# Kernel optimization log

Measured on AMD Instinct MI355X. Metric: run time of the kernel, lower is better.

The kernel has to match this reference:

```python
import jax, jax.numpy as jnp
import numpy as np
from jax import lax

LR, SB, LB = 256, 16, 8  # lr_size, spatial_bin, luma_bins
DN = ('NCHW', 'OIHW', 'NCHW')


def conv2d(x, w, b=None, stride=1, pad=1):
    out = lax.conv_general_dilated(x, w, (stride, stride), [(pad, pad), (pad, pad)], dimension_numbers=DN)
    return out if b is None else out + b[None, :, None, None]


def gaussian_blur17(x):
    # kornia GaussianBlur2d(kernel=(17,17), sigma=(2,2)), reflect padding, separable
    t = jnp.arange(17, dtype=x.dtype) - 8.0
    g = jnp.exp(-(t * t) / 8.0)  # 2*sigma^2 = 8
    g = g / g.sum()
    C = x.shape[1]
    xp = jnp.pad(x, ((0, 0), (0, 0), (8, 8), (8, 8)), mode='reflect')
    kh = jnp.broadcast_to(g.reshape(1, 1, 17, 1), (C, 1, 17, 1))
    kw = jnp.broadcast_to(g.reshape(1, 1, 1, 17), (C, 1, 1, 17))
    x1 = lax.conv_general_dilated(xp, kh, (1, 1), 'VALID', dimension_numbers=DN, feature_group_count=C)
    return lax.conv_general_dilated(x1, kw, (1, 1), 'VALID', dimension_numbers=DN, feature_group_count=C)


def nearest_resize(x, size):
    # torch F.interpolate mode='nearest': src = floor(dst * in/out)
    H, W = x.shape[-2], x.shape[-1]
    iy = jnp.floor(jnp.arange(size) * (H / size)).astype(jnp.int32)
    ix = jnp.floor(jnp.arange(size) * (W / size)).astype(jnp.int32)
    return x[:, :, iy][:, :, :, ix]


def grid_sample_3d_border(inp, grid):
    # inp [B,C,D,Hi,Wi]; grid [B,Do,Ho,Wo,3] with (x,y,z); bilinear, padding_mode='border', align_corners=False
    B, C, D, Hi, Wi = inp.shape
    x = jnp.clip(((grid[..., 0] + 1.0) * Wi - 1.0) * 0.5, 0.0, Wi - 1.0)
    y = jnp.clip(((grid[..., 1] + 1.0) * Hi - 1.0) * 0.5, 0.0, Hi - 1.0)
    z = jnp.clip(((grid[..., 2] + 1.0) * D - 1.0) * 0.5, 0.0, D - 1.0)
    x0 = jnp.floor(x); y0 = jnp.floor(y); z0 = jnp.floor(z)
    fx = (x - x0)[:, None]; fy = (y - y0)[:, None]; fz = (z - z0)[:, None]  # [B,1,Do,Ho,Wo]
    x0i = x0.astype(jnp.int32); y0i = y0.astype(jnp.int32); z0i = z0.astype(jnp.int32)
    x1i = jnp.minimum(x0i + 1, Wi - 1); y1i = jnp.minimum(y0i + 1, Hi - 1); z1i = jnp.minimum(z0i + 1, D - 1)
    flat = inp.reshape(B, C, D * Hi * Wi)
    M = grid.shape[1] * grid.shape[2] * grid.shape[3]

    def gat(zi, yi, xi):
        idx = ((zi * Hi + yi) * Wi + xi).reshape(B, 1, M)
        v = jnp.take_along_axis(flat, jnp.broadcast_to(idx, (B, C, M)), axis=2)
        return v.reshape(B, C, grid.shape[1], grid.shape[2], grid.shape[3])

    return (gat(z0i, y0i, x0i) * (1 - fz) * (1 - fy) * (1 - fx)
            + gat(z0i, y0i, x1i) * (1 - fz) * (1 - fy) * fx
            + gat(z0i, y1i, x0i) * (1 - fz) * fy * (1 - fx)
            + gat(z0i, y1i, x1i) * (1 - fz) * fy * fx
            + gat(z1i, y0i, x0i) * fz * (1 - fy) * (1 - fx)
            + gat(z1i, y0i, x1i) * fz * (1 - fy) * fx
            + gat(z1i, y1i, x0i) * fz * fy * (1 - fx)
            + gat(z1i, y1i, x1i) * fz * fy * fx)


def _forward(lqs, evs, gw1, gb1, gw2, gb2, sw0, sb0, sw1, sb1, sw2, sb2, sw3, sb3,
             cw0, cb0, cw1, cb1, fw1, fb1, fw2, fb2, fw3, fb3, lw1, lb1, lw2, fuw, fub):
    B, _, H, W = lqs.shape
    # --- HighresStreamNet guide ---
    g = gaussian_blur17(lqs)
    g = jax.nn.relu(conv2d(g, gw1, gb1, 1, 0))
    guide = jax.nn.sigmoid(conv2d(g, gw2, gb2, 1, 0)) * 2.0 - 0.5  # [B,1,H,W]
    # --- slicing grid (x,y in (-0.5,1.5) per source, z = guide) ---
    gx = (jnp.arange(W, dtype=lqs.dtype) + 0.5) / W * 2.0 - 0.5
    gy = (jnp.arange(H, dtype=lqs.dtype) + 0.5) / H * 2.0 - 0.5
    gyy, gxx = jnp.meshgrid(gy, gx, indexing='ij')
    base = jnp.broadcast_to(jnp.stack([gxx, gyy], -1)[None, None], (B, 1, H, W, 2))
    grid = jnp.concatenate([base, guide[..., None]], axis=-1)  # [B,1,H,W,3]
    # --- LowresStreamNet ---
    lr = nearest_resize(lqs, LR)
    ev = evs if (evs.shape[-1] == LR and evs.shape[-2] == LR) else nearest_resize(evs, LR)
    x = jnp.concatenate([lr, ev], axis=1)  # [B,18,256,256]
    for w_, b_ in ((sw0, sb0), (sw1, sb1), (sw2, sb2), (sw3, sb3)):
        x = jax.nn.relu(conv2d(x, w_, b_, 2, 1))  # -> [B,64,16,16]
    xl = conv2d(jax.nn.relu(conv2d(x, lw1, lb1, 1, 1)), lw2, None, 1, 1)  # local, last conv no bias
    xg = jax.nn.relu(conv2d(x, cw0, cb0, 2, 1))
    xg = jax.nn.relu(conv2d(xg, cw1, cb1, 2, 1)).reshape(B, -1)  # [B,1024]
    xg = jax.nn.relu(xg @ fw1.T + fb1)
    xg = jax.nn.relu(xg @ fw2.T + fb2)
    xg = xg @ fw3.T + fb3  # [B,64]
    fused = jax.nn.relu(xg[:, :, None, None] + xl)
    bg = conv2d(fused, fuw, fub, 1, 0).reshape(B, 1, LB, SB, SB)  # bilateral grid [B,1,8,16,16]
    hr = grid_sample_3d_border(bg, grid)  # [B,1,1,H,W]
    return hr.reshape(B, -1, H, W)


def setup_inputs():
    key = jax.random.key(0)
    ks = iter(jax.random.split(key, 40))

    def W_(shape):
        fan_in = int(np.prod(shape[1:]))
        return jax.random.normal(next(ks), shape, jnp.float32) * np.float32(np.sqrt(2.0 / fan_in))

    def Z(n):
        return jnp.zeros((n,), jnp.float32)

    B, H, Wd = 8, 1024, 1024
    return {
        'lqs': jax.random.uniform(next(ks), (B, 3, H, Wd), jnp.float32),
        'evs': jax.random.normal(next(ks), (B, 15, 256, 256), jnp.float32) * 0.1,
        'gw1': W_((16, 3, 1, 1)), 'gb1': Z(16), 'gw2': W_((1, 16, 1, 1)), 'gb2': Z(1),
        'sw0': W_((8, 18, 3, 3)), 'sb0': Z(8), 'sw1': W_((16, 8, 3, 3)), 'sb1': Z(16),
        'sw2': W_((32, 16, 3, 3)), 'sb2': Z(32), 'sw3': W_((64, 32, 3, 3)), 'sb3': Z(64),
        'cw0': W_((64, 64, 3, 3)), 'cb0': Z(64), 'cw1': W_((64, 64, 3, 3)), 'cb1': Z(64),
        'fw1': W_((256, 1024)), 'fb1': Z(256), 'fw2': W_((128, 256)), 'fb2': Z(128),
        'fw3': W_((64, 128)), 'fb3': Z(64),
        'lw1': W_((64, 64, 3, 3)), 'lb1': Z(64), 'lw2': W_((64, 64, 3, 3)),
        'fuw': W_((8, 64, 1, 1)), 'fub': Z(8),
    }


def reference(lqs, evs, gw1, gb1, gw2, gb2, sw0, sb0, sw1, sb1, sw2, sb2, sw3, sb3,
              cw0, cb0, cw1, cb1, fw1, fb1, fw2, fb2, fw3, fb3, lw1, lb1, lw2, fuw, fub):
    return _forward(lqs, evs, gw1, gb1, gw2, gb2, sw0, sb0, sw1, sb1, sw2, sb2, sw3, sb3,
                    cw0, cb0, cw1, cb1, fw1, fb1, fw2, fb2, fw3, fb3, lw1, lb1, lw2, fuw, fub)
```

## Files before the change

### kernel.cpp

```cpp
#include <hip/hip_runtime.h>
#include <hip/hip_bf16.h>
#include <math.h>

#define BATCH 8
#define HH 1024
#define WW 1024

__device__ __forceinline__ int reflect1024(int i) {
    i = i < 0 ? -i : i;
    return i > 1023 ? 2046 - i : i;
}

__global__ __launch_bounds__(256) void conv01_k(const float* __restrict__ lqs,
                                                const float* __restrict__ evs,
                                                const float* __restrict__ sw0,
                                                const float* __restrict__ sb0,
                                                const float* __restrict__ sw1,
                                                const float* __restrict__ sb1,
                                                float* __restrict__ o1) {
    __shared__ float s0[8 * 81];
    int t = threadIdx.x;
    int blk = blockIdx.x;
    int tx = blk & 15, ty = (blk >> 4) & 15, b = blk >> 8;
    int oy0 = ty << 2, ox0 = tx << 2;
    int iy0s = 2 * oy0 - 1, ix0s = 2 * ox0 - 1;

    if (t < 81) {
        int p = t;
        int yy = p / 9, xx = p - yy * 9;
        int iy = iy0s + yy, ix = ix0s + xx;
        if ((unsigned)iy < 128u && (unsigned)ix < 128u) {
            float acc[8];
#pragma unroll
            for (int o = 0; o < 8; ++o) acc[o] = sb0[o];
#pragma unroll
            for (int ic = 0; ic < 3; ++ic) {
                const float* ipc = lqs + ((size_t)(b * 3 + ic) << 20);
#pragma unroll
                for (int ky = 0; ky < 3; ++ky) {
                    int r = 2 * iy - 1 + ky;
                    if ((unsigned)r >= 256u) continue;
                    const float* row = ipc + ((size_t)r << 12);
#pragma unroll
                    for (int kx = 0; kx < 3; ++kx) {
                        int c = 2 * ix - 1 + kx;
                        if ((unsigned)c >= 256u) continue;
                        float v = row[c << 2];
                        const float* wp = sw0 + ic * 9 + ky * 3 + kx;
#pragma unroll
                        for (int o = 0; o < 8; ++o) acc[o] = fmaf(wp[o * 162], v, acc[o]);
                    }
                }
            }
            for (int ic = 0; ic < 15; ++ic) {
                const float* ipc = evs + ((size_t)(b * 15 + ic) << 16);
#pragma unroll
                for (int ky = 0; ky < 3; ++ky) {
                    int r = 2 * iy - 1 + ky;
                    if ((unsigned)r >= 256u) continue;
                    const float* row = ipc + (r << 8);
#pragma unroll
                    for (int kx = 0; kx < 3; ++kx) {
                        int c = 2 * ix - 1 + kx;
                        if ((unsigned)c >= 256u) continue;
                        float v = row[c];
                        const float* wp = sw0 + (ic + 3) * 9 + ky * 3 + kx;
#pragma unroll
                        for (int o = 0; o < 8; ++o) acc[o] = fmaf(wp[o * 162], v, acc[o]);
                    }
                }
            }
#pragma unroll
            for (int o = 0; o < 8; ++o) s0[o * 81 + p] = fmaxf(acc[o], 0.0f);
        } else {
#pragma unroll
            for (int o = 0; o < 8; ++o) s0[o * 81 + p] = 0.0f;
        }
    }
    __syncthreads();

    int px = t & 15, oc = t >> 4;
    int lpy = px >> 2, lpx = px & 3;
    float a1 = sb1[oc];
#pragma unroll
    for (int ic = 0; ic < 8; ++ic) {
        const float* sp = s0 + ic * 81 + (2 * lpy) * 9 + 2 * lpx;
        float x[9];
#pragma unroll
        for (int ky = 0; ky < 3; ++ky)
#pragma unroll
            for (int kx = 0; kx < 3; ++kx) x[ky * 3 + kx] = sp[ky * 9 + kx];
        const float* wp = sw1 + (oc * 8 + ic) * 9;
#pragma unroll
        for (int k = 0; k < 9; ++k) a1 = fmaf(wp[k], x[k], a1);
    }
    int oy = oy0 + lpy, ox = ox0 + lpx;
    o1[((size_t)(b * 16 + oc) << 12) + (oy << 6) + ox] = fmaxf(a1, 0.0f);
}

__global__ __launch_bounds__(256) void conv23_k(const float* __restrict__ o1,
                                                const float* __restrict__ sw2,
                                                const float* __restrict__ sb2,
                                                const float* __restrict__ sw3,
                                                const float* __restrict__ sb3,
                                                float* __restrict__ o3) {
    __shared__ float s2[32 * 25];
    int t = threadIdx.x;
    int blk = blockIdx.x;
    int tx = blk & 7, ty = (blk >> 3) & 7, b = blk >> 6;
    int oy0 = ty << 1, ox0 = tx << 1;
    int iy0s = 2 * oy0 - 1, ix0s = 2 * ox0 - 1;

    if (t < 100) {
        int ocg = t / 25, p = t - ocg * 25;
        int yy = p / 5, xx = p - yy * 5;
        int iy = iy0s + yy, ix = ix0s + xx;
        if ((unsigned)iy < 32u && (unsigned)ix < 32u) {
            float acc[8];
#pragma unroll
            for (int o = 0; o < 8; ++o) acc[o] = sb2[ocg * 8 + o];
            const float* ip = o1 + ((size_t)b << 16);
            int ry0 = 2 * iy - 1, rx0 = 2 * ix - 1;
            for (int ic = 0; ic < 16; ++ic) {
                const float* ipc = ip + (ic << 12);
                float x[9];
#pragma unroll
                for (int ky = 0; ky < 3; ++ky) {
                    int r = ry0 + ky;
#pragma unroll
                    for (int kx = 0; kx < 3; ++kx) {
                        int c = rx0 + kx;
                        bool ok = ((unsigned)r < 64u) && ((unsigned)c < 64u);
                        x[ky * 3 + kx] = ok ? ipc[(r << 6) + c] : 0.0f;
                    }
                }
#pragma unroll
                for (int o = 0; o < 8; ++o) {
                    const float* wp = sw2 + ((ocg * 8 + o) * 16 + ic) * 9;
#pragma unroll
                    for (int k = 0; k < 9; ++k) acc[o] = fmaf(wp[k], x[k], acc[o]);
                }
            }
#pragma unroll
            for (int o = 0; o < 8; ++o) s2[(ocg * 8 + o) * 25 + p] = fmaxf(acc[o], 0.0f);
        } else {
#pragma unroll
            for (int o = 0; o < 8; ++o) s2[(ocg * 8 + o) * 25 + p] = 0.0f;
        }
    }
    __syncthreads();

    int oc = t >> 2, p2 = t & 3;
    int py = p2 >> 1, pxx = p2 & 1;
    float a3 = sb3[oc];
    for (int ic = 0; ic < 32; ++ic) {
        const float* wp = sw3 + (oc * 32 + ic) * 9;
        const float* sp = s2 + ic * 25 + (2 * py) * 5 + 2 * pxx;
#pragma unroll
        for (int ky = 0; ky < 3; ++ky)
#pragma unroll
            for (int kx = 0; kx < 3; ++kx)
                a3 = fmaf(wp[ky * 3 + kx], sp[ky * 5 + kx], a3);
    }
    o3[((size_t)(b * 64 + oc) << 8) + ((oy0 + py) << 4) + (ox0 + pxx)] = fmaxf(a3, 0.0f);
}

__global__ __launch_bounds__(256) void lw1cw0_k(const float* __restrict__ o3,
                                                const float* __restrict__ lw1,
                                                const float* __restrict__ lb1,
                                                const float* __restrict__ cw0,
                                                const float* __restrict__ cb0,
                                                float* __restrict__ xl1,
                                                float* __restrict__ xg0) {
    __shared__ float sW[2304];
    int blk = blockIdx.x, t = threadIdx.x;
    if (blk < 512) {
        int b = blk >> 6, oc = blk & 63;
        for (int i = t; i < 576; i += 256) sW[i] = lw1[oc * 576 + i];
        __syncthreads();
        int oy = t >> 4, ox = t & 15;
        int iy0 = oy - 1, ix0 = ox - 1;
        float acc = lb1[oc];
        const float* ip = o3 + ((size_t)b << 14);
        for (int ic = 0; ic < 64; ++ic) {
            const float* ipc = ip + (ic << 8);
            float x[9];
#pragma unroll
            for (int ky = 0; ky < 3; ++ky) {
                int iy = iy0 + ky;
#pragma unroll
                for (int kx = 0; kx < 3; ++kx) {
                    int ix = ix0 + kx;
                    bool ok = ((unsigned)iy < 16u) && ((unsigned)ix < 16u);
                    x[ky * 3 + kx] = ok ? ipc[(iy << 4) + ix] : 0.0f;
                }
            }
            const float* wp = sW + ic * 9;
#pragma unroll
            for (int k = 0; k < 9; ++k) acc = fmaf(wp[k], x[k], acc);
        }
        xl1[((size_t)(b * 64 + oc) << 8) + t] = fmaxf(acc, 0.0f);
    } else {
        int q = blk - 512;
        int b = q >> 4, oc_base = (q & 15) << 2;
        for (int i = t; i < 2304; i += 256) sW[i] = cw0[oc_base * 576 + i];
        __syncthreads();
        int px = t & 63, ol = t >> 6;
        int oy = px >> 3, ox = px & 7;
        int iy0 = 2 * oy - 1, ix0 = 2 * ox - 1;
        float acc = cb0[oc_base + ol];
        const float* ip = o3 + ((size_t)b << 14);
        for (int ic = 0; ic < 64; ++ic) {
            const float* ipc = ip + (ic << 8);
            float x[9];
#pragma unroll
            for (int ky = 0; ky < 3; ++ky) {
                int iy = iy0 + ky;
#pragma unroll
                for (int kx = 0; kx < 3; ++kx) {
                    int ix = ix0 + kx;
                    bool ok = ((unsigned)iy < 16u) && ((unsigned)ix < 16u);
                    x[ky * 3 + kx] = ok ? ipc[(iy << 4) + ix] : 0.0f;
                }
            }
            const float* wp = sW + ol * 576 + ic * 9;
#pragma unroll
            for (int k = 0; k < 9; ++k) acc = fmaf(wp[k], x[k], acc);
        }
        xg0[((size_t)(b * 64 + oc_base + ol) << 6) + px] = fmaxf(acc, 0.0f);
    }
}

__global__ __launch_bounds__(256) void lw2cw1fc1_k(const float* __restrict__ xl1,
                                                   const float* __restrict__ lw2,
                                                   const float* __restrict__ xg0,
                                                   const float* __restrict__ cw1,
                                                   const float* __restrict__ cb1,
                                                   const float* __restrict__ fw1,
                                                   const float* __restrict__ fb1,
                                                   float* __restrict__ xl2,
                                                   float* __restrict__ h1) {
    __shared__ __align__(16) float smem[14336];
    int blk = blockIdx.x, t = threadIdx.x;
    if (blk < 512) {
        float* sW = smem;
        int b = blk >> 6, oc = blk & 63;
        for (int i = t; i < 576; i += 256) sW[i] = lw2[oc * 576 + i];
        __syncthreads();
        int oy = t >> 4, ox = t & 15;
        int iy0 = oy - 1, ix0 = ox - 1;
        float acc = 0.0f;
        const float* ip = xl1 + ((size_t)b << 14);
        for (int ic = 0; ic < 64; ++ic) {
            const float* ipc = ip + (ic << 8);
            float x[9];
#pragma unroll
            for (int ky = 0; ky < 3; ++ky) {
                int iy = iy0 + ky;
#pragma unroll
                for (int kx = 0; kx < 3; ++kx) {
                    int ix = ix0 + kx;
                    bool ok = ((unsigned)iy < 16u) && ((unsigned)ix < 16u);
                    x[ky * 3 + kx] = ok ? ipc[(iy << 4) + ix] : 0.0f;
                }
            }
            const float* wp = sW + ic * 9;
#pragma unroll
            for (int k = 0; k < 9; ++k) acc = fmaf(wp[k], x[k], acc);
        }
        xl2[((size_t)(b * 64 + oc) << 8) + t] = acc;
        return;
    }
    int q = blk - 512;
    int b = q >> 3, rg = q & 7;
    float* sG  = smem;
    float* sX  = smem + 4096;
    float* sWc = smem + 5120;

#pragma unroll
    for (int j = 0; j < 16; ++j) sG[t + (j << 8)] = xg0[((size_t)b << 12) + t + (j << 8)];
    __syncthreads();

    for (int c = 0; c < 4; ++c) {
        for (int i = t; i < 9216; i += 256) sWc[i] = cw1[c * 9216 + i];
        __syncthreads();
        int ol = t >> 4, px = t & 15;
        int oc = (c << 4) + ol;
        int oy = px >> 2, ox = px & 3;
        int iy0 = 2 * oy - 1, ix0 = 2 * ox - 1;
        float acc = cb1[oc];
        for (int ic = 0; ic < 64; ++ic) {
            const float* ipc = sG + (ic << 6);
            const float* wp = sWc + ol * 576 + ic * 9;
#pragma unroll
            for (int ky = 0; ky < 3; ++ky) {
                int r = iy0 + ky;
#pragma unroll
                for (int kx = 0; kx < 3; ++kx) {
                    int cc = ix0 + kx;
                    bool ok = ((unsigned)r < 8u) && ((unsigned)cc < 8u);
                    float x = ok ? ipc[(r << 3) + cc] : 0.0f;
                    acc = fmaf(wp[ky * 3 + kx], x, acc);
                }
            }
        }
        sX[(oc << 4) + px] = fmaxf(acc, 0.0f);
        __syncthreads();
    }

    int wave = t >> 6, lane = t & 63;
    const float4* x4 = (const float4*)sX;
#pragma unroll
    for (int k = 0; k < 8; ++k) {
        int r = (rg << 5) + (wave << 3) + k;
        const float4* w4 = (const float4*)(fw1 + (size_t)r * 1024);
        float acc = 0.0f;
#pragma unroll
        for (int jj = 0; jj < 4; ++jj) {
            float4 wv = w4[lane + 64 * jj];
            float4 xv = x4[lane + 64 * jj];
            acc = fmaf(wv.x, xv.x, acc);
            acc = fmaf(wv.y, xv.y, acc);
            acc = fmaf(wv.z, xv.z, acc);
            acc = fmaf(wv.w, xv.w, acc);
        }
#pragma unroll
        for (int m = 32; m; m >>= 1) acc += __shfl_xor(acc, m, 64);
        if (lane == 0) h1[b * 256 + r] = fmaxf(acc + fb1[r], 0.0f);
    }
}

__global__ __launch_bounds__(256) void bgfuse_k(const float* __restrict__ h1g,
                                                const float* __restrict__ fw2,
                                                const float* __restrict__ fb2,
                                                const float* __restrict__ fw3,
                                                const float* __restrict__ fb3,
                                                const float* __restrict__ xl2,
                                                const float* __restrict__ fuw,
                                                const float* __restrict__ fub,
                                                float* __restrict__ bg) {
    __shared__ __align__(16) float sH1[256];
    __shared__ __align__(16) float sH2[128];
    __shared__ float sXG[64];
    int b = blockIdx.x, t = threadIdx.x;

    sH1[t] = h1g[b * 256 + t];
    __syncthreads();

    if (t < 128) {
        const float4* w4 = (const float4*)(fw2 + (size_t)t * 256);
        const float4* x4 = (const float4*)sH1;
        float a[4] = {0.f, 0.f, 0.f, 0.f};
#pragma unroll 4
        for (int j = 0; j < 64; ++j) {
            float4 wv = w4[j], xv = x4[j];
            a[j & 3] = fmaf(wv.x, xv.x, fmaf(wv.y, xv.y,
                       fmaf(wv.z, xv.z, fmaf(wv.w, xv.w, a[j & 3]))));
        }
        sH2[t] = fmaxf(a[0] + a[1] + a[2] + a[3] + fb2[t], 0.0f);
    }
    __syncthreads();
    if (t < 64) {
        const float4* w4 = (const float4*)(fw3 + (size_t)t * 128);
        const float4* x4 = (const float4*)sH2;
        float a[4] = {0.f, 0.f, 0.f, 0.f};
#pragma unroll 4
        for (int j = 0; j < 32; ++j) {
            float4 wv = w4[j], xv = x4[j];
            a[j & 3] = fmaf(wv.x, xv.x, fmaf(wv.y, xv.y,
                       fmaf(wv.z, xv.z, fmaf(wv.w, xv.w, a[j & 3]))));
        }
        sXG[t] = a[0] + a[1] + a[2] + a[3] + fb3[t];
    }
    __syncthreads();

    float accd[8];
#pragma unroll
    for (int d = 0; d < 8; ++d) accd[d] = fub[d];
    const float* xp = xl2 + ((size_t)b << 14) + t;
    for (int c = 0; c < 64; ++c) {
        float f = fmaxf(sXG[c] + xp[c << 8], 0.0f);
#pragma unroll
        for (int d = 0; d < 8; ++d) accd[d] = fmaf(fuw[(d << 6) + c], f, accd[d]);
    }
#pragma unroll
    for (int d = 0; d < 8; ++d) bg[((b << 3) + d) * 256 + t] = accd[d];
}

__global__ __launch_bounds__(256) void guide_slice_k(const float* __restrict__ lqs,
                                                     const float* __restrict__ bgp,
                                                     const float* __restrict__ gw1,
                                                     const float* __restrict__ gb1,
                                                     const float* __restrict__ gw2,
                                                     const float* __restrict__ gb2,
                                                     float* __restrict__ out) {
    constexpr int TW = 64, TH = 16;
    __shared__ float sBH[3][TH][81];
    __shared__ float sBG[2048];
    __shared__ float sW1[48], sB1[16], sW2[16], sB2v[1];

    int t = threadIdx.x;
    int bx = blockIdx.x & 15;
    int by = (blockIdx.x >> 4) & 63;
    int b = blockIdx.x >> 10;
    int x0 = bx * TW, y0 = by * TH;

    float gv[17];
    {
        float gs = 0.0f;
#pragma unroll
        for (int i = 0; i < 17; ++i) {
            float d = (float)i - 8.0f;
            gv[i] = expf(-(d * d) * 0.125f);
            gs += gv[i];
        }
        float inv = 1.0f / gs;
#pragma unroll
        for (int i = 0; i < 17; ++i) gv[i] *= inv;
    }

    for (int i = t; i < 2048; i += 256) sBG[i] = bgp[b * 2048 + i];
    if (t < 48) sW1[t] = gw1[t];
    if (t < 16) { sB1[t] = gb1[t]; sW2[t] = gw2[t]; }
    if (t == 0) sB2v[0] = gb2[0];

    if (t < 240) {
        int c = t / 80, xo = t % 80;
        int gx = reflect1024(x0 + xo - 8);
        const float* colp = lqs + (size_t)(b * 3 + c) * HH * WW + gx;
        float win[17];
#pragma unroll
        for (int i = 0; i < 16; ++i)
            win[i] = colp[(size_t)reflect1024(y0 - 8 + i) * WW];
#pragma unroll
        for (int j = 0; j < TH; ++j) {
            win[(16 + j) % 17] = colp[(size_t)reflect1024(y0 + 8 + j) * WW];
            float acc = 0.0f;
#pragma unroll
            for (int i = 0; i < 17; ++i) acc = fmaf(gv[i], win[(j + i) % 17], acc);
            sBH[c][j][xo] = acc;
        }
    }
    __syncthreads();

    int yy = t >> 4, xs = (t & 15) * 4;
    int Y = y0 + yy;
    float fy = fminf(fmaxf((Y + 0.5f) * (1.0f / 64.0f) + 3.5f, 0.0f), 15.0f);
    float yf = floorf(fy);
    int yi = (int)yf;
    float ay = fy - yf;
    int yi1 = min(yi + 1, 15);

    float bcv[3][4];
#pragma unroll
    for (int c = 0; c < 3; ++c) {
        float win[17];
#pragma unroll
        for (int i = 0; i < 16; ++i) win[i] = sBH[c][yy][xs + i];
#pragma unroll
        for (int j = 0; j < 4; ++j) {
            win[(16 + j) % 17] = sBH[c][yy][xs + 16 + j];
            float acc = 0.0f;
#pragma unroll
            for (int i = 0; i < 17; ++i) acc = fmaf(gv[i], win[(j + i) % 17], acc);
            bcv[c][j] = acc;
        }
    }

    float val[4];
#pragma unroll
    for (int j = 0; j < 4; ++j) {
        float b0 = bcv[0][j], b1 = bcv[1][j], b2 = bcv[2][j];
        float s = sB2v[0];
#pragma unroll
        for (int c = 0; c < 16; ++c) {
            float g1 = fmaf(sW1[c * 3 + 0], b0,
                       fmaf(sW1[c * 3 + 1], b1,
                       fmaf(sW1[c * 3 + 2], b2, sB1[c])));
            s = fmaf(sW2[c], fmaxf(g1, 0.0f), s);
        }
        float sig = 1.0f / (1.0f + expf(-s));
        float guide = sig * 2.0f - 0.5f;

        int X = x0 + xs + j;
        float fx = fminf(fmaxf((X + 0.5f) * (1.0f / 64.0f) + 3.5f, 0.0f), 15.0f);
        float fz = fminf(fmaxf(fmaf(guide, 4.0f, 3.5f), 0.0f), 7.0f);
        float xf = floorf(fx), zf = floorf(fz);
        int xi = (int)xf, zi = (int)zf;
        float ax = fx - xf, az = fz - zf;
        int xi1 = min(xi + 1, 15), zi1 = min(zi + 1, 7);

        const float* g0 = sBG + zi * 256;
        const float* g1p = sBG + zi1 * 256;
        int i00 = yi * 16 + xi, i01 = yi * 16 + xi1;
        int i10 = yi1 * 16 + xi, i11 = yi1 * 16 + xi1;
        float c00 = g0[i00] + az * (g1p[i00] - g0[i00]);
        float c01 = g0[i01] + az * (g1p[i01] - g0[i01]);
        float c10 = g0[i10] + az * (g1p[i10] - g0[i10]);
        float c11 = g0[i11] + az * (g1p[i11] - g0[i11]);
        float c0 = c00 + ay * (c10 - c00);
        float c1 = c01 + ay * (c11 - c01);
        val[j] = c0 + ax * (c1 - c0);
    }
    float4* op = (float4*)(out + (size_t)b * HH * WW + (size_t)Y * WW + x0 + xs);
    op[0] = make_float4(val[0], val[1], val[2], val[3]);
}

extern "C" void kernel_launch(void* const* d_in, const int* in_sizes, int n_in,
                              void* d_out, int out_size, void* d_ws, size_t ws_size,
                              hipStream_t stream) {
    const float* lqs = (const float*)d_in[0];
    const float* evs = (const float*)d_in[1];
    const float* gw1 = (const float*)d_in[2];
    const float* gb1 = (const float*)d_in[3];
    const float* gw2 = (const float*)d_in[4];
    const float* gb2 = (const float*)d_in[5];
    const float* sw0 = (const float*)d_in[6];
    const float* sb0 = (const float*)d_in[7];
    const float* sw1 = (const float*)d_in[8];
    const float* sb1 = (const float*)d_in[9];
    const float* sw2 = (const float*)d_in[10];
    const float* sb2 = (const float*)d_in[11];
    const float* sw3 = (const float*)d_in[12];
    const float* sb3 = (const float*)d_in[13];
    const float* cw0 = (const float*)d_in[14];
    const float* cb0 = (const float*)d_in[15];
    const float* cw1 = (const float*)d_in[16];
    const float* cb1 = (const float*)d_in[17];
    const float* fw1 = (const float*)d_in[18];
    const float* fb1 = (const float*)d_in[19];
    const float* fw2 = (const float*)d_in[20];
    const float* fb2 = (const float*)d_in[21];
    const float* fw3 = (const float*)d_in[22];
    const float* fb3 = (const float*)d_in[23];
    const float* lw1 = (const float*)d_in[24];
    const float* lb1 = (const float*)d_in[25];
    const float* lw2 = (const float*)d_in[26];
    const float* fuw = (const float*)d_in[27];
    const float* fub = (const float*)d_in[28];
    float* out = (float*)d_out;

    float* ws = (float*)d_ws;
    float* o1  = ws;
    float* o3  = o1 + 524288;
    float* xl1 = o3 + 131072;
    float* xl2 = xl1 + 131072;
    float* xg0 = xl2 + 131072;
    float* h1  = xg0 + 32768;
    float* bg  = h1 + 2048;

    conv01_k<<<2048, 256, 0, stream>>>(lqs, evs, sw0, sb0, sw1, sb1, o1);
    conv23_k<<<512, 256, 0, stream>>>(o1, sw2, sb2, sw3, sb3, o3);
    lw1cw0_k<<<640, 256, 0, stream>>>(o3, lw1, lb1, cw0, cb0, xl1, xg0);
    lw2cw1fc1_k<<<576, 256, 0, stream>>>(xl1, lw2, xg0, cw1, cb1, fw1, fb1, xl2, h1);
    bgfuse_k<<<8, 256, 0, stream>>>(h1, fw2, fb2, fw3, fb3, xl2, fuw, fub, bg);
    guide_slice_k<<<BATCH * 64 * 16, 256, 0, stream>>>(lqs, bg, gw1, gb1, gw2, gb2, out);
}
```

Measured before the change: 468.1 us.

## Compute cw1 conv once per batch and move fc1 into the bgfuse kernel

Previously each of 8 row-group blocks per batch recomputed the full cw1 conv before doing its slice of fc1. Now 64 blocks each compute 8 output channels of cw1 once and write xg1 to global memory, and the fc1 layer moves into the 8-block bgfuse kernel. This removes the 8x redundant conv work. The cost is that fc1 now runs on only 8 blocks, so each reads all 1 MB of fw1 weights with little parallelism. The cw1 weight tile in shared memory is padded to a 584 stride to reduce bank conflicts.

```diff
diff --git a/kernel.cpp b/kernel.cpp
--- a/kernel.cpp
+++ b/kernel.cpp
@@ -231,20 +231,53 @@
     }
 }
 
-__global__ __launch_bounds__(256) void lw2cw1fc1_k(const float* __restrict__ xl1,
-                                                   const float* __restrict__ lw2,
-                                                   const float* __restrict__ xg0,
-                                                   const float* __restrict__ cw1,
-                                                   const float* __restrict__ cb1,
-                                                   const float* __restrict__ fw1,
-                                                   const float* __restrict__ fb1,
-                                                   float* __restrict__ xl2,
-                                                   float* __restrict__ h1) {
-    __shared__ __align__(16) float smem[14336];
+__global__ __launch_bounds__(256) void lw2cw1_k(const float* __restrict__ xl1,
+                                                const float* __restrict__ lw2,
+                                                const float* __restrict__ xg0,
+                                                const float* __restrict__ cw1,
+                                                const float* __restrict__ cb1,
+                                                float* __restrict__ xl2,
+                                                float* __restrict__ xg1) {
+    __shared__ __align__(16) float smem[8768];
     int blk = blockIdx.x, t = threadIdx.x;
-    if (blk < 512) {
+    if (blk < 64) {
+        int b = blk >> 3, og = blk & 7;
+        float* sG = smem;
+        float* sW = smem + 4096;
+#pragma unroll
+        for (int j = 0; j < 16; ++j) sG[t + (j << 8)] = xg0[((size_t)b << 12) + t + (j << 8)];
+        for (int i = t; i < 4608; i += 256) {
+            int ol = i / 576, r = i - ol * 576;
+            sW[ol * 584 + r] = cw1[(og * 8 + ol) * 576 + r];
+        }
+        __syncthreads();
+        if (t < 128) {
+            int ol = t >> 4, px = t & 15;
+            int oc = og * 8 + ol;
+            int oy = px >> 2, ox = px & 3;
+            int iy0 = 2 * oy - 1, ix0 = 2 * ox - 1;
+            float acc = cb1[oc];
+            for (int ic = 0; ic < 64; ++ic) {
+                const float* ipc = sG + (ic << 6);
+                const float* wp = sW + ol * 584 + ic * 9;
+#pragma unroll
+                for (int ky = 0; ky < 3; ++ky) {
+                    int r = iy0 + ky;
+#pragma unroll
+                    for (int kx = 0; kx < 3; ++kx) {
+                        int cc = ix0 + kx;
+                        bool ok = ((unsigned)r < 8u) && ((unsigned)cc < 8u);
+                        float x = ok ? ipc[(r << 3) + cc] : 0.0f;
+                        acc = fmaf(wp[ky * 3 + kx], x, acc);
+                    }
+                }
+            }
+            xg1[b * 1024 + (oc << 4) + px] = fmaxf(acc, 0.0f);
+        }
+    } else {
+        int q = blk - 64;
         float* sW = smem;
-        int b = blk >> 6, oc = blk & 63;
+        int b = q >> 6, oc = q & 63;
         for (int i = t; i < 576; i += 256) sW[i] = lw2[oc * 576 + i];
         __syncthreads();
         int oy = t >> 4, ox = t & 15;
@@ -269,82 +302,51 @@
             for (int k = 0; k < 9; ++k) acc = fmaf(wp[k], x[k], acc);
         }
         xl2[((size_t)(b * 64 + oc) << 8) + t] = acc;
-        return;
-    }
-    int q = blk - 512;
-    int b = q >> 3, rg = q & 7;
-    float* sG  = smem;
-    float* sX  = smem + 4096;
-    float* sWc = smem + 5120;
-
-#pragma unroll
-    for (int j = 0; j < 16; ++j) sG[t + (j << 8)] = xg0[((size_t)b << 12) + t + (j << 8)];
-    __syncthreads();
-
-    for (int c = 0; c < 4; ++c) {
-        for (int i = t; i < 9216; i += 256) sWc[i] = cw1[c * 9216 + i];
-        __syncthreads();
-        int ol = t >> 4, px = t & 15;
-        int oc = (c << 4) + ol;
-        int oy = px >> 2, ox = px & 3;
-        int iy0 = 2 * oy - 1, ix0 = 2 * ox - 1;
-        float acc = cb1[oc];
-        for (int ic = 0; ic < 64; ++ic) {
-            const float* ipc = sG + (ic << 6);
-            const float* wp = sWc + ol * 576 + ic * 9;
-#pragma unroll
-            for (int ky = 0; ky < 3; ++ky) {
-                int r = iy0 + ky;
-#pragma unroll
-                for (int kx = 0; kx < 3; ++kx) {
-                    int cc = ix0 + kx;
-                    bool ok = ((unsigned)r < 8u) && ((unsigned)cc < 8u);
-                    float x = ok ? ipc[(r << 3) + cc] : 0.0f;
-                    acc = fmaf(wp[ky * 3 + kx], x, acc);
-                }
-            }
-        }
-        sX[(oc << 4) + px] = fmaxf(acc, 0.0f);
-        __syncthreads();
-    }
-
-    int wave = t >> 6, lane = t & 63;
-    const float4* x4 = (const float4*)sX;
-#pragma unroll
-    for (int k = 0; k < 8; ++k) {
-        int r = (rg << 5) + (wave << 3) + k;
-        const float4* w4 = (const float4*)(fw1 + (size_t)r * 1024);
-        float acc = 0.0f;
-#pragma unroll
-        for (int jj = 0; jj < 4; ++jj) {
-            float4 wv = w4[lane + 64 * jj];
-            float4 xv = x4[lane + 64 * jj];
-            acc = fmaf(wv.x, xv.x, acc);
-            acc = fmaf(wv.y, xv.y, acc);
-            acc = fmaf(wv.z, xv.z, acc);
-            acc = fmaf(wv.w, xv.w, acc);
-        }
-#pragma unroll
-        for (int m = 32; m; m >>= 1) acc += __shfl_xor(acc, m, 64);
-        if (lane == 0) h1[b * 256 + r] = fmaxf(acc + fb1[r], 0.0f);
-    }
-}
-
-__global__ __launch_bounds__(256) void bgfuse_k(const float* __restrict__ h1g,
-                                                const float* __restrict__ fw2,
-                                                const float* __restrict__ fb2,
-                                                const float* __restrict__ fw3,
-                                                const float* __restrict__ fb3,
-                                                const float* __restrict__ xl2,
-                                                const float* __restrict__ fuw,
-                                                const float* __restrict__ fub,
-                                                float* __restrict__ bg) {
+    }
+}
+
+__global__ __launch_bounds__(256) void fc1bgfuse_k(const float* __restrict__ xg1,
+                                                   const float* __restrict__ fw1,
+                                                   const float* __restrict__ fb1,
+                                                   const float* __restrict__ fw2,
+                                                   const float* __restrict__ fb2,
+                                                   const float* __restrict__ fw3,
+                                                   const float* __restrict__ fb3,
+                                                   const float* __restrict__ xl2,
+                                                   const float* __restrict__ fuw,
+                                                   const float* __restrict__ fub,
+                                                   float* __restrict__ bg) {
+    __shared__ __align__(16) float sX[1024];
     __shared__ __align__(16) float sH1[256];
     __shared__ __align__(16) float sH2[128];
     __shared__ float sXG[64];
     int b = blockIdx.x, t = threadIdx.x;
 
-    sH1[t] = h1g[b * 256 + t];
+#pragma unroll
+    for (int j = 0; j < 4; ++j) sX[t + (j << 8)] = xg1[b * 1024 + t + (j << 8)];
+    __syncthreads();
+
+    {
+        int wave = t >> 6, lane = t & 63;
+        const float4* x4 = (const float4*)sX;
+        for (int k = 0; k < 64; ++k) {
+            int r = (wave << 6) + k;
+            const float4* w4 = (const float4*)(fw1 + (size_t)r * 1024);
+            float acc = 0.0f;
+#pragma unroll
+            for (int jj = 0; jj < 4; ++jj) {
+                float4 wv = w4[lane + 64 * jj];
+                float4 xv = x4[lane + 64 * jj];
+                acc = fmaf(wv.x, xv.x, acc);
+                acc = fmaf(wv.y, xv.y, acc);
+                acc = fmaf(wv.z, xv.z, acc);
+                acc = fmaf(wv.w, xv.w, acc);
+            }
+#pragma unroll
+            for (int m = 32; m; m >>= 1) acc += __shfl_xor(acc, m, 64);
+            if (lane == 0) sH1[r] = fmaxf(acc + fb1[r], 0.0f);
+        }
+    }
     __syncthreads();
 
     if (t < 128) {
@@ -546,13 +548,14 @@
     float* xl1 = o3 + 131072;
     float* xl2 = xl1 + 131072;
     float* xg0 = xl2 + 131072;
-    float* h1  = xg0 + 32768;
-    float* bg  = h1 + 2048;
+    float* xg1 = xg0 + 32768;
+    float* bg  = xg1 + 8192;
 
     conv01_k<<<2048, 256, 0, stream>>>(lqs, evs, sw0, sb0, sw1, sb1, o1);
     conv23_k<<<512, 256, 0, stream>>>(o1, sw2, sb2, sw3, sb3, o3);
     lw1cw0_k<<<640, 256, 0, stream>>>(o3, lw1, lb1, cw0, cb0, xl1, xg0);
-    lw2cw1fc1_k<<<576, 256, 0, stream>>>(xl1, lw2, xg0, cw1, cb1, fw1, fb1, xl2, h1);
-    bgfuse_k<<<8, 256, 0, stream>>>(h1, fw2, fb2, fw3, fb3, xl2, fuw, fub, bg);
+    lw2cw1_k<<<576, 256, 0, stream>>>(xl1, lw2, xg0, cw1, cb1, xl2, xg1);
+    fc1bgfuse_k<<<8, 256, 0, stream>>>(xg1, fw1, fb1, fw2, fb2, fw3, fb3,
+                                       xl2, fuw, fub, bg);
     guide_slice_k<<<BATCH * 64 * 16, 256, 0, stream>>>(lqs, bg, gw1, gb1, gw2, gb2, out);
 }
```

New measurement: 467.2 us. Within noise of the previous version (-0.2%).
